# Performance work log

Hardware: AMD Instinct MI355X
Metric: run time of the kernel (lower is better)

Reference implementation:

```python
import jax, jax.numpy as jnp
import numpy as np
from jax import lax

NPOINT, RADIUS, NSAMPLE, K_KEY = 64, 1.0, 32, 64

def conv1d(x, W, b):
    # 1x1 Conv1d: x [B,Cin,N], W [Cout,Cin], b [Cout] -> [B,Cout,N]
    return jnp.einsum('bcn,dc->bdn', x, W) + b[None, :, None]

def farthest_point_sample(xyz, npoint):
    # xyz [B,N,3] -> idx [B,npoint]
    B, N, _ = xyz.shape
    dist0 = jnp.full((B, N), 1e10, dtype=xyz.dtype)
    far0 = jnp.zeros((B,), dtype=jnp.int32)
    def body(carry, _):
        dist, far = carry
        centroid = jnp.take_along_axis(xyz, far[:, None, None].astype(jnp.int32), axis=1)  # [B,1,3]
        d = jnp.sum((xyz - centroid) ** 2, -1)
        dist = jnp.minimum(dist, d)
        nxt = jnp.argmax(dist, -1).astype(jnp.int32)
        return (dist, nxt), far
    _, idxs = lax.scan(body, (dist0, far0), None, length=npoint)
    return idxs.T  # [B,npoint]

def ball_query(radius, nsample, xyz, new_xyz):
    # xyz [B,N,3], new_xyz [B,S,3] -> group_idx [B,S,nsample]
    N = xyz.shape[1]
    sqr = jnp.sum((new_xyz[:, :, None, :] - xyz[:, None, :, :]) ** 2, -1)  # [B,S,N]
    gidx = jnp.where(sqr > radius ** 2, N, jnp.arange(N, dtype=jnp.int32)[None, None, :])
    gidx = jnp.sort(gidx, axis=-1)[..., :nsample]
    first = gidx[..., :1]
    gidx = jnp.where(gidx == N, first, gidx)
    return gidx

def sample_and_group(npoint, radius, nsample, xyz, points):
    # xyz [B,N,3], points [B,N,D]
    B = xyz.shape[0]
    fps_idx = farthest_point_sample(xyz, npoint)                     # [B,S]
    bidx = jnp.arange(B)[:, None]
    new_xyz = xyz[bidx, fps_idx]                                     # [B,S,3]
    gidx = ball_query(radius, nsample, xyz, new_xyz)                 # [B,S,ns]
    bidx2 = jnp.arange(B)[:, None, None]
    grouped_xyz = xyz[bidx2, gidx]                                   # [B,S,ns,3]
    grouped_xyz_norm = grouped_xyz - new_xyz[:, :, None, :]
    grouped_points = points[bidx2, gidx]                             # [B,S,ns,D]
    new_points = jnp.concatenate([grouped_xyz_norm, grouped_points], axis=-1)
    return new_xyz, new_points

def setup_inputs() -> dict:
    key = jax.random.key(0)
    ks = jax.random.split(key, 12)
    B, C, N = 8, 6, 65536
    def w(k, co, ci):
        return jax.random.normal(k, (co, ci), jnp.float32) * (1.0 / np.sqrt(ci))
    return {
        'src_pts': jax.random.normal(ks[0], (B, C, N), jnp.float32),
        'tgt_pts': jax.random.normal(ks[1], (B, C, N), jnp.float32),
        'W1': w(ks[2], 32, 6),  'b1': jnp.zeros((32,), jnp.float32),
        'W2': w(ks[3], 64, 32), 'b2': jnp.zeros((64,), jnp.float32),
        'Wa': w(ks[4], 16, 64), 'ba': jnp.zeros((16,), jnp.float32),
        'Wb': w(ks[5], 8, 16),  'bb': jnp.zeros((8,), jnp.float32),
        'Wc': w(ks[6], 1, 8),   'bc': jnp.zeros((1,), jnp.float32),
    }

def reference(src_pts, tgt_pts, W1, b1, W2, b2, Wa, ba, Wb, bb, Wc, bc):
    # feat_extraction_layer: 1x1 conv stack over points -> deep per-point features
    h = jax.nn.relu(conv1d(src_pts, W1, b1))            # [B,32,N]
    deep_feat_pts = jax.nn.relu(conv1d(h, W2, b2))      # [B,64,N]
    # weighting_layer: per-point saliency weight + top-k keypoint indices (1-D, batch-0 idiom)
    w = jax.nn.relu(conv1d(deep_feat_pts, Wa, ba))
    w = jax.nn.relu(conv1d(w, Wb, bb))
    w = jax.nn.softplus(conv1d(w, Wc, bc))              # [B,1,N]
    _, keypts_idx = lax.top_k(w[0, 0], K_KEY)           # [K]
    # irregular keypoint gather (shared index across batch, as in src_pts[:, :, idx])
    src_keypts = src_pts[:, :, keypts_idx].transpose(0, 2, 1)   # [B,K,C]
    # ball-query sample_and_group on keypoints (computed then discarded, as in original)
    _gxyz, _gpts = sample_and_group(NPOINT, RADIUS, NSAMPLE, src_keypts[:, :, :3], src_keypts[:, :, 3:])
    return src_keypts
```

## Files before the change

kernel.cpp:

```cpp
#include <hip/hip_runtime.h>
#include <stdint.h>

#define N_PTS 65536
#define NB1 32768
#define NB2 65536
#define CAND_CAP 4096
typedef unsigned long long u64;


__global__ __launch_bounds__(256) void zero_kernel(unsigned* __restrict__ z, int n)
{
    const int i = blockIdx.x * 256 + threadIdx.x;
    if (i < n) z[i] = 0u;
}

__global__ __launch_bounds__(256, 1) void score_kernel(
    const float* __restrict__ src,
    const float* __restrict__ W1, const float* __restrict__ b1,
    const float* __restrict__ W2, const float* __restrict__ b2,
    const float* __restrict__ Wa, const float* __restrict__ ba,
    const float* __restrict__ Wb, const float* __restrict__ bb,
    const float* __restrict__ Wc, const float* __restrict__ bc,
    float* __restrict__ scores, unsigned* __restrict__ hist1)
{
    __shared__ unsigned histL[NB1];
    __shared__ __align__(16) float sW1[32 * 8];
    __shared__ __align__(16) float sW2[64 * 32];
    __shared__ __align__(16) float sWaT[64 * 16];
    __shared__ __align__(16) float sWb[8 * 16];
    __shared__ float sb2[64], sba[16], sbb[8], sWc[8], sbc1[1];
    const int t = threadIdx.x;

    {
        uint4* h4 = (uint4*)histL;
        const uint4 zz = {0u, 0u, 0u, 0u};
        #pragma unroll
        for (int i = 0; i < 32; i++) h4[t + 256 * i] = zz;
    }

    {
        const int j = t >> 3, c = t & 7;
        sW1[t] = (c < 6) ? W1[j * 6 + c] : ((c == 6) ? b1[j] : 0.f);
    }
    for (int i = t; i < 2048; i += 256) sW2[i] = W2[i];
    for (int i = t; i < 1024; i += 256) {
        const int j = i >> 4, q = i & 15;
        sWaT[i] = Wa[q * 64 + j];
    }
    if (t < 128) sWb[t] = Wb[t];
    if (t < 64)  sb2[t] = b2[t];
    if (t < 16)  sba[t] = ba[t];
    if (t < 8)   { sbb[t] = bb[t]; sWc[t] = Wc[t]; }
    if (t == 0)  sbc1[0] = bc[0];
    __syncthreads();

    const int p = blockIdx.x * 256 + t;
    float x0 = src[0 * N_PTS + p], x1 = src[1 * N_PTS + p];
    float x2 = src[2 * N_PTS + p], x3 = src[3 * N_PTS + p];
    float x4 = src[4 * N_PTS + p], x5 = src[5 * N_PTS + p];

    float h1[32];
    #pragma unroll
    for (int j = 0; j < 32; j++) {
        const float4 wA = *(const float4*)&sW1[j * 8];
        const float4 wB = *(const float4*)&sW1[j * 8 + 4];
        float a = wB.z;
        a = fmaf(wA.x, x0, a); a = fmaf(wA.y, x1, a);
        a = fmaf(wA.z, x2, a); a = fmaf(wA.w, x3, a);
        a = fmaf(wB.x, x4, a); a = fmaf(wB.y, x5, a);
        h1[j] = fmaxf(a, 0.f);
    }

    float h3[16];
    #pragma unroll
    for (int q = 0; q < 16; q++) h3[q] = sba[q];

    #pragma unroll 4
    for (int j = 0; j < 64; j++) {
        const float4* w2r = (const float4*)&sW2[j * 32];
        float a0 = 0.f, a1 = 0.f, a2 = 0.f, a3 = 0.f;
        #pragma unroll
        for (int i4 = 0; i4 < 8; i4++) {
            const float4 w = w2r[i4];
            a0 = fmaf(w.x, h1[4 * i4 + 0], a0);
            a1 = fmaf(w.y, h1[4 * i4 + 1], a1);
            a2 = fmaf(w.z, h1[4 * i4 + 2], a2);
            a3 = fmaf(w.w, h1[4 * i4 + 3], a3);
        }
        const float v = fmaxf((a0 + a1) + (a2 + a3) + sb2[j], 0.f);
        const float4* war = (const float4*)&sWaT[j * 16];
        #pragma unroll
        for (int q4 = 0; q4 < 4; q4++) {
            const float4 w = war[q4];
            h3[4 * q4 + 0] = fmaf(w.x, v, h3[4 * q4 + 0]);
            h3[4 * q4 + 1] = fmaf(w.y, v, h3[4 * q4 + 1]);
            h3[4 * q4 + 2] = fmaf(w.z, v, h3[4 * q4 + 2]);
            h3[4 * q4 + 3] = fmaf(w.w, v, h3[4 * q4 + 3]);
        }
    }
    #pragma unroll
    for (int q = 0; q < 16; q++) h3[q] = fmaxf(h3[q], 0.f);

    float z = sbc1[0];
    #pragma unroll
    for (int j = 0; j < 8; j++) {
        const float4* wbr = (const float4*)&sWb[j * 16];
        const float4 wA = wbr[0], wB = wbr[1], wC = wbr[2], wD = wbr[3];
        float s0 = sbb[j], s1 = 0.f, s2 = 0.f, s3 = 0.f;
        s0 = fmaf(wA.x, h3[0],  s0); s1 = fmaf(wA.y, h3[1],  s1);
        s2 = fmaf(wA.z, h3[2],  s2); s3 = fmaf(wA.w, h3[3],  s3);
        s0 = fmaf(wB.x, h3[4],  s0); s1 = fmaf(wB.y, h3[5],  s1);
        s2 = fmaf(wB.z, h3[6],  s2); s3 = fmaf(wB.w, h3[7],  s3);
        s0 = fmaf(wC.x, h3[8],  s0); s1 = fmaf(wC.y, h3[9],  s1);
        s2 = fmaf(wC.z, h3[10], s2); s3 = fmaf(wC.w, h3[11], s3);
        s0 = fmaf(wD.x, h3[12], s0); s1 = fmaf(wD.y, h3[13], s1);
        s2 = fmaf(wD.z, h3[14], s2); s3 = fmaf(wD.w, h3[15], s3);
        z = fmaf(sWc[j], fmaxf((s0 + s1) + (s2 + s3), 0.f), z);
    }

    const float sp = fmaxf(z, 0.f) + log1pf(expf(-fabsf(z)));
    scores[p] = sp;
    atomicAdd(&histL[__float_as_uint(sp) >> 16], 1u);
    __syncthreads();

    for (int i = t; i < NB1; i += 256) {
        const unsigned v = histL[i];
        if (v) atomicAdd(&hist1[i], v);
    }
}

__global__ __launch_bounds__(256) void refine_kernel(
    const unsigned* __restrict__ hist1, const float* __restrict__ scores,
    unsigned* __restrict__ hist2, int* __restrict__ meta)
{
    __shared__ unsigned csum[256];
    __shared__ unsigned bsum[128];
    __shared__ int sh_c, sh_B;
    __shared__ unsigned sh_tail;
    const int t = threadIdx.x;

    {
        unsigned s = 0;
        const uint4* h4 = (const uint4*)(hist1 + t * 128);
        #pragma unroll
        for (int i = 0; i < 32; i++) {
            const uint4 v = h4[i];
            s += v.x + v.y + v.z + v.w;
        }
        csum[t] = s;
    }
    __syncthreads();
    for (int d = 1; d < 256; d <<= 1) {
        const unsigned v = (t + d < 256) ? csum[t + d] : 0u;
        __syncthreads();
        csum[t] += v;
        __syncthreads();
    }
    {
        const unsigned here = csum[t];
        const unsigned nxt = (t + 1 < 256) ? csum[t + 1] : 0u;
        if (here >= 64u && nxt < 64u) sh_c = t;
    }
    __syncthreads();
    const int cstar = sh_c;
    if (t < 128) bsum[t] = hist1[cstar * 128 + t];
    __syncthreads();
    {
        const unsigned ctail = (cstar + 1 < 256) ? csum[cstar + 1] : 0u;
        for (int d = 1; d < 128; d <<= 1) {
            unsigned v = 0u;
            if (t < 128 && t + d < 128) v = bsum[t + d];
            __syncthreads();
            if (t < 128) bsum[t] += v;
            __syncthreads();
        }
        if (t < 128) {
            const unsigned here = bsum[t] + ctail;
            const unsigned nxt = (t + 1 < 128) ? bsum[t + 1] + ctail : ctail;
            if (here >= 64u && nxt < 64u) { sh_B = cstar * 128 + t; sh_tail = nxt; }
        }
    }
    __syncthreads();
    const unsigned Bstar = (unsigned)sh_B;
    if (blockIdx.x == 0 && t == 0) { meta[0] = sh_B; meta[1] = (int)sh_tail; }

    const float4* s4 = (const float4*)scores;
    const int i = blockIdx.x * 256 + t;
    const float4 v = s4[i];
    unsigned b;
    b = __float_as_uint(v.x); if ((b >> 16) == Bstar) atomicAdd(&hist2[b & 0xFFFFu], 1u);
    b = __float_as_uint(v.y); if ((b >> 16) == Bstar) atomicAdd(&hist2[b & 0xFFFFu], 1u);
    b = __float_as_uint(v.z); if ((b >> 16) == Bstar) atomicAdd(&hist2[b & 0xFFFFu], 1u);
    b = __float_as_uint(v.w); if ((b >> 16) == Bstar) atomicAdd(&hist2[b & 0xFFFFu], 1u);
}

__global__ __launch_bounds__(256) void compact_kernel(
    const unsigned* __restrict__ hist2, const float* __restrict__ scores,
    int* __restrict__ meta, u64* __restrict__ cand)
{
    __shared__ unsigned csum[256];
    __shared__ unsigned bsum[256];
    __shared__ int sh_c, sh_T2;
    const int t = threadIdx.x;
    const unsigned Bstar = (unsigned)meta[0];
    const unsigned tail1 = (unsigned)meta[1];

    {
        unsigned s = 0;
        const uint4* h4 = (const uint4*)(hist2 + t * 256);
        #pragma unroll
        for (int i = 0; i < 64; i++) {
            const uint4 v = h4[i];
            s += v.x + v.y + v.z + v.w;
        }
        csum[t] = s;
    }
    __syncthreads();
    for (int d = 1; d < 256; d <<= 1) {
        const unsigned v = (t + d < 256) ? csum[t + d] : 0u;
        __syncthreads();
        csum[t] += v;
        __syncthreads();
    }
    {
        const unsigned here = tail1 + csum[t];
        const unsigned nxt = tail1 + ((t + 1 < 256) ? csum[t + 1] : 0u);
        if (here >= 64u && nxt < 64u) sh_c = t;
    }
    __syncthreads();
    const int cstar = sh_c;
    bsum[t] = hist2[cstar * 256 + t];
    __syncthreads();
    {
        const unsigned ctail = tail1 + ((cstar + 1 < 256) ? csum[cstar + 1] : 0u);
        for (int d = 1; d < 256; d <<= 1) {
            const unsigned v = (t + d < 256) ? bsum[t + d] : 0u;
            __syncthreads();
            bsum[t] += v;
            __syncthreads();
        }
        const unsigned here = bsum[t] + ctail;
        const unsigned nxt = ((t + 1 < 256) ? bsum[t + 1] : 0u) + ctail;
        if (here >= 64u && nxt < 64u) sh_T2 = cstar * 256 + t;
    }
    __syncthreads();
    const unsigned T2 = (unsigned)sh_T2;

    const float4* s4 = (const float4*)scores;
    const int i = blockIdx.x * 256 + t;
    const float4 v = s4[i];
    const int n0 = 4 * i;
    unsigned b; unsigned hi;
    b = __float_as_uint(v.x); hi = b >> 16;
    if (hi > Bstar || (hi == Bstar && (b & 0xFFFFu) >= T2)) { int p = atomicAdd(&meta[2], 1); if (p < CAND_CAP) cand[p] = ((u64)b << 32) | (unsigned)~(n0 + 0); }
    b = __float_as_uint(v.y); hi = b >> 16;
    if (hi > Bstar || (hi == Bstar && (b & 0xFFFFu) >= T2)) { int p = atomicAdd(&meta[2], 1); if (p < CAND_CAP) cand[p] = ((u64)b << 32) | (unsigned)~(n0 + 1); }
    b = __float_as_uint(v.z); hi = b >> 16;
    if (hi > Bstar || (hi == Bstar && (b & 0xFFFFu) >= T2)) { int p = atomicAdd(&meta[2], 1); if (p < CAND_CAP) cand[p] = ((u64)b << 32) | (unsigned)~(n0 + 2); }
    b = __float_as_uint(v.w); hi = b >> 16;
    if (hi > Bstar || (hi == Bstar && (b & 0xFFFFu) >= T2)) { int p = atomicAdd(&meta[2], 1); if (p < CAND_CAP) cand[p] = ((u64)b << 32) | (unsigned)~(n0 + 3); }
}

__global__ __launch_bounds__(256) void final_kernel(
    const int* __restrict__ meta, const u64* __restrict__ cand,
    const float* __restrict__ src, float* __restrict__ out)
{
    __shared__ u64 keys[CAND_CAP];
    __shared__ int idxs[64];
    const int t = threadIdx.x;

    int count = meta[2];
    if (count > CAND_CAP) count = CAND_CAP;

    for (int i = t; i < count; i += 256) keys[i] = cand[i];
    __syncthreads();

    for (int i = t; i < count; i += 256) {
        const u64 me = keys[i];
        int r = 0;
        for (int j = 0; j < count; j++) r += (keys[j] > me);
        if (r < 64) idxs[r] = (int)~(unsigned)(me & 0xFFFFFFFFu);
    }
    __syncthreads();

    for (int e = t; e < 3072; e += 256) {
        const int b  = e / 384;
        const int rr = e % 384;
        const int kk = rr / 6;
        const int c  = rr % 6;
        out[e] = src[(b * 6 + c) * N_PTS + idxs[kk]];
    }
}

extern "C" void kernel_launch(void* const* d_in, const int* in_sizes, int n_in,
                              void* d_out, int out_size, void* d_ws, size_t ws_size,
                              hipStream_t stream)
{
    const float* src = (const float*)d_in[0];
    const float* W1 = (const float*)d_in[2];
    const float* b1 = (const float*)d_in[3];
    const float* W2 = (const float*)d_in[4];
    const float* b2 = (const float*)d_in[5];
    const float* Wa = (const float*)d_in[6];
    const float* ba = (const float*)d_in[7];
    const float* Wb = (const float*)d_in[8];
    const float* bb = (const float*)d_in[9];
    const float* Wc = (const float*)d_in[10];
    const float* bc = (const float*)d_in[11];

    char* ws = (char*)d_ws;
    float*    scores = (float*)ws;
    unsigned* hist1  = (unsigned*)(ws + 256 * 1024);
    unsigned* hist2  = (unsigned*)(ws + 384 * 1024);
    int*      meta   = (int*)(ws + 640 * 1024);
    u64*      cand   = (u64*)(ws + 640 * 1024 + 64);
    float*    out    = (float*)d_out;

    const int nz = NB1 + NB2 + 16;
    zero_kernel<<<(nz + 255) / 256, 256, 0, stream>>>(hist1, nz);
    score_kernel<<<256, 256, 0, stream>>>(src, W1, b1, W2, b2, Wa, ba,
                                          Wb, bb, Wc, bc, scores, hist1);
    refine_kernel<<<64, 256, 0, stream>>>(hist1, scores, hist2, meta);
    compact_kernel<<<64, 256, 0, stream>>>(hist2, scores, meta, cand);
    final_kernel<<<1, 256, 0, stream>>>(meta, cand, src, out);
}
```

Baseline: 145.5 us.

## Fuse refine, compact and final into one last-block select kernel; two points per thread

Merges the refine, compact and final top-k kernels into a single select kernel. Blocks build the second-level histogram, and the last block to finish (found through an atomic done counter) computes the threshold, compacts candidates into shared memory, ranks them and gathers the output. The score kernel now runs 128 threads per block with two points per thread, so each shared-memory weight load is reused across both points. This removes two kernel launches and the global candidate buffer, but the final scan over all scores now runs in one block and the candidate cap shrinks to 2048.

```diff
diff --git a/kernel.cpp b/kernel.cpp
--- a/kernel.cpp
+++ b/kernel.cpp
@@ -4,17 +4,18 @@
 #define N_PTS 65536
 #define NB1 32768
 #define NB2 65536
-#define CAND_CAP 4096
+#define LCAP 2048
 typedef unsigned long long u64;
 
 
-__global__ __launch_bounds__(256) void zero_kernel(unsigned* __restrict__ z, int n)
+__global__ __launch_bounds__(256) void zero_kernel(uint4* __restrict__ z, int n4)
 {
     const int i = blockIdx.x * 256 + threadIdx.x;
-    if (i < n) z[i] = 0u;
+    const uint4 zz = {0u, 0u, 0u, 0u};
+    if (i < n4) z[i] = zz;
 }
 
-__global__ __launch_bounds__(256, 1) void score_kernel(
+__global__ __launch_bounds__(128, 1) void score_kernel(
     const float* __restrict__ src,
     const float* __restrict__ W1, const float* __restrict__ b1,
     const float* __restrict__ W2, const float* __restrict__ b2,
@@ -35,15 +36,14 @@
         uint4* h4 = (uint4*)histL;
         const uint4 zz = {0u, 0u, 0u, 0u};
         #pragma unroll
-        for (int i = 0; i < 32; i++) h4[t + 256 * i] = zz;
-    }
-
-    {
-        const int j = t >> 3, c = t & 7;
-        sW1[t] = (c < 6) ? W1[j * 6 + c] : ((c == 6) ? b1[j] : 0.f);
-    }
-    for (int i = t; i < 2048; i += 256) sW2[i] = W2[i];
-    for (int i = t; i < 1024; i += 256) {
+        for (int i = 0; i < 64; i++) h4[t + 128 * i] = zz;
+    }
+    for (int i = t; i < 256; i += 128) {
+        const int j = i >> 3, c = i & 7;
+        sW1[i] = (c < 6) ? W1[j * 6 + c] : ((c == 6) ? b1[j] : 0.f);
+    }
+    for (int i = t; i < 2048; i += 128) sW2[i] = W2[i];
+    for (int i = t; i < 1024; i += 128) {
         const int j = i >> 4, q = i & 15;
         sWaT[i] = Wa[q * 64 + j];
     }
@@ -54,89 +54,118 @@
     if (t == 0)  sbc1[0] = bc[0];
     __syncthreads();
 
-    const int p = blockIdx.x * 256 + t;
-    float x0 = src[0 * N_PTS + p], x1 = src[1 * N_PTS + p];
-    float x2 = src[2 * N_PTS + p], x3 = src[3 * N_PTS + p];
-    float x4 = src[4 * N_PTS + p], x5 = src[5 * N_PTS + p];
-
-    float h1[32];
+    const int base = blockIdx.x * 256;
+    const int p[2] = { base + t, base + 128 + t };
+
+    float x[2][6];
+    #pragma unroll
+    for (int c = 0; c < 6; c++) {
+        x[0][c] = src[c * N_PTS + p[0]];
+        x[1][c] = src[c * N_PTS + p[1]];
+    }
+
+    float h1[2][32];
     #pragma unroll
     for (int j = 0; j < 32; j++) {
         const float4 wA = *(const float4*)&sW1[j * 8];
         const float4 wB = *(const float4*)&sW1[j * 8 + 4];
-        float a = wB.z;
-        a = fmaf(wA.x, x0, a); a = fmaf(wA.y, x1, a);
-        a = fmaf(wA.z, x2, a); a = fmaf(wA.w, x3, a);
-        a = fmaf(wB.x, x4, a); a = fmaf(wB.y, x5, a);
-        h1[j] = fmaxf(a, 0.f);
-    }
-
-    float h3[16];
-    #pragma unroll
-    for (int q = 0; q < 16; q++) h3[q] = sba[q];
+        #pragma unroll
+        for (int P = 0; P < 2; P++) {
+            float a = wB.z;
+            a = fmaf(wA.x, x[P][0], a); a = fmaf(wA.y, x[P][1], a);
+            a = fmaf(wA.z, x[P][2], a); a = fmaf(wA.w, x[P][3], a);
+            a = fmaf(wB.x, x[P][4], a); a = fmaf(wB.y, x[P][5], a);
+            h1[P][j] = fmaxf(a, 0.f);
+        }
+    }
+
+    float h3[2][16];
+    #pragma unroll
+    for (int q = 0; q < 16; q++) { h3[0][q] = sba[q]; h3[1][q] = sba[q]; }
 
     #pragma unroll 4
     for (int j = 0; j < 64; j++) {
         const float4* w2r = (const float4*)&sW2[j * 32];
-        float a0 = 0.f, a1 = 0.f, a2 = 0.f, a3 = 0.f;
-        #pragma unroll
-        for (int i4 = 0; i4 < 8; i4++) {
-            const float4 w = w2r[i4];
-            a0 = fmaf(w.x, h1[4 * i4 + 0], a0);
-            a1 = fmaf(w.y, h1[4 * i4 + 1], a1);
-            a2 = fmaf(w.z, h1[4 * i4 + 2], a2);
-            a3 = fmaf(w.w, h1[4 * i4 + 3], a3);
-        }
-        const float v = fmaxf((a0 + a1) + (a2 + a3) + sb2[j], 0.f);
+        float4 w[8];
+        #pragma unroll
+        for (int i = 0; i < 8; i++) w[i] = w2r[i];
+        const float bj = sb2[j];
         const float4* war = (const float4*)&sWaT[j * 16];
-        #pragma unroll
-        for (int q4 = 0; q4 < 4; q4++) {
-            const float4 w = war[q4];
-            h3[4 * q4 + 0] = fmaf(w.x, v, h3[4 * q4 + 0]);
-            h3[4 * q4 + 1] = fmaf(w.y, v, h3[4 * q4 + 1]);
-            h3[4 * q4 + 2] = fmaf(w.z, v, h3[4 * q4 + 2]);
-            h3[4 * q4 + 3] = fmaf(w.w, v, h3[4 * q4 + 3]);
-        }
-    }
-    #pragma unroll
-    for (int q = 0; q < 16; q++) h3[q] = fmaxf(h3[q], 0.f);
-
-    float z = sbc1[0];
+        float4 wq[4];
+        #pragma unroll
+        for (int i = 0; i < 4; i++) wq[i] = war[i];
+        #pragma unroll
+        for (int P = 0; P < 2; P++) {
+            float a0 = 0.f, a1 = 0.f, a2 = 0.f, a3 = 0.f;
+            #pragma unroll
+            for (int i4 = 0; i4 < 8; i4++) {
+                a0 = fmaf(w[i4].x, h1[P][4 * i4 + 0], a0);
+                a1 = fmaf(w[i4].y, h1[P][4 * i4 + 1], a1);
+                a2 = fmaf(w[i4].z, h1[P][4 * i4 + 2], a2);
+                a3 = fmaf(w[i4].w, h1[P][4 * i4 + 3], a3);
+            }
+            const float v = fmaxf((a0 + a1) + (a2 + a3) + bj, 0.f);
+            #pragma unroll
+            for (int q4 = 0; q4 < 4; q4++) {
+                h3[P][4 * q4 + 0] = fmaf(wq[q4].x, v, h3[P][4 * q4 + 0]);
+                h3[P][4 * q4 + 1] = fmaf(wq[q4].y, v, h3[P][4 * q4 + 1]);
+                h3[P][4 * q4 + 2] = fmaf(wq[q4].z, v, h3[P][4 * q4 + 2]);
+                h3[P][4 * q4 + 3] = fmaf(wq[q4].w, v, h3[P][4 * q4 + 3]);
+            }
+        }
+    }
+    #pragma unroll
+    for (int q = 0; q < 16; q++) {
+        h3[0][q] = fmaxf(h3[0][q], 0.f);
+        h3[1][q] = fmaxf(h3[1][q], 0.f);
+    }
+
+    float z[2] = { sbc1[0], sbc1[0] };
     #pragma unroll
     for (int j = 0; j < 8; j++) {
         const float4* wbr = (const float4*)&sWb[j * 16];
-        const float4 wA = wbr[0], wB = wbr[1], wC = wbr[2], wD = wbr[3];
-        float s0 = sbb[j], s1 = 0.f, s2 = 0.f, s3 = 0.f;
-        s0 = fmaf(wA.x, h3[0],  s0); s1 = fmaf(wA.y, h3[1],  s1);
-        s2 = fmaf(wA.z, h3[2],  s2); s3 = fmaf(wA.w, h3[3],  s3);
-        s0 = fmaf(wB.x, h3[4],  s0); s1 = fmaf(wB.y, h3[5],  s1);
-        s2 = fmaf(wB.z, h3[6],  s2); s3 = fmaf(wB.w, h3[7],  s3);
-        s0 = fmaf(wC.x, h3[8],  s0); s1 = fmaf(wC.y, h3[9],  s1);
-        s2 = fmaf(wC.z, h3[10], s2); s3 = fmaf(wC.w, h3[11], s3);
-        s0 = fmaf(wD.x, h3[12], s0); s1 = fmaf(wD.y, h3[13], s1);
-        s2 = fmaf(wD.z, h3[14], s2); s3 = fmaf(wD.w, h3[15], s3);
-        z = fmaf(sWc[j], fmaxf((s0 + s1) + (s2 + s3), 0.f), z);
-    }
-
-    const float sp = fmaxf(z, 0.f) + log1pf(expf(-fabsf(z)));
-    scores[p] = sp;
-    atomicAdd(&histL[__float_as_uint(sp) >> 16], 1u);
-    __syncthreads();
-
-    for (int i = t; i < NB1; i += 256) {
+        const float4 w0 = wbr[0], w1 = wbr[1], w2 = wbr[2], w3 = wbr[3];
+        const float bj = sbb[j], wc = sWc[j];
+        #pragma unroll
+        for (int P = 0; P < 2; P++) {
+            float s0 = bj, s1 = 0.f, s2 = 0.f, s3 = 0.f;
+            s0 = fmaf(w0.x, h3[P][0],  s0); s1 = fmaf(w0.y, h3[P][1],  s1);
+            s2 = fmaf(w0.z, h3[P][2],  s2); s3 = fmaf(w0.w, h3[P][3],  s3);
+            s0 = fmaf(w1.x, h3[P][4],  s0); s1 = fmaf(w1.y, h3[P][5],  s1);
+            s2 = fmaf(w1.z, h3[P][6],  s2); s3 = fmaf(w1.w, h3[P][7],  s3);
+            s0 = fmaf(w2.x, h3[P][8],  s0); s1 = fmaf(w2.y, h3[P][9],  s1);
+            s2 = fmaf(w2.z, h3[P][10], s2); s3 = fmaf(w2.w, h3[P][11], s3);
+            s0 = fmaf(w3.x, h3[P][12], s0); s1 = fmaf(w3.y, h3[P][13], s1);
+            s2 = fmaf(w3.z, h3[P][14], s2); s3 = fmaf(w3.w, h3[P][15], s3);
+            z[P] = fmaf(wc, fmaxf((s0 + s1) + (s2 + s3), 0.f), z[P]);
+        }
+    }
+
+    #pragma unroll
+    for (int P = 0; P < 2; P++) {
+        const float sp = fmaxf(z[P], 0.f) + log1pf(expf(-fabsf(z[P])));
+        scores[p[P]] = sp;
+        atomicAdd(&histL[__float_as_uint(sp) >> 16], 1u);
+    }
+    __syncthreads();
+
+    for (int i = t; i < NB1; i += 128) {
         const unsigned v = histL[i];
         if (v) atomicAdd(&hist1[i], v);
     }
 }
 
-__global__ __launch_bounds__(256) void refine_kernel(
+__global__ __launch_bounds__(256) void select_kernel(
     const unsigned* __restrict__ hist1, const float* __restrict__ scores,
-    unsigned* __restrict__ hist2, int* __restrict__ meta)
+    unsigned* __restrict__ hist2, unsigned* __restrict__ done,
+    const float* __restrict__ src, float* __restrict__ out)
 {
     __shared__ unsigned csum[256];
-    __shared__ unsigned bsum[128];
-    __shared__ int sh_c, sh_B;
-    __shared__ unsigned sh_tail;
+    __shared__ unsigned bsum[256];
+    __shared__ u64 keys[LCAP];
+    __shared__ int idxs[64];
+    __shared__ int sh_c, sh_B, sh_T2, sh_cnt;
+    __shared__ unsigned sh_tail, sh_rank;
     const int t = threadIdx.x;
 
     {
@@ -182,28 +211,25 @@
     }
     __syncthreads();
     const unsigned Bstar = (unsigned)sh_B;
-    if (blockIdx.x == 0 && t == 0) { meta[0] = sh_B; meta[1] = (int)sh_tail; }
-
-    const float4* s4 = (const float4*)scores;
-    const int i = blockIdx.x * 256 + t;
-    const float4 v = s4[i];
-    unsigned b;
-    b = __float_as_uint(v.x); if ((b >> 16) == Bstar) atomicAdd(&hist2[b & 0xFFFFu], 1u);
-    b = __float_as_uint(v.y); if ((b >> 16) == Bstar) atomicAdd(&hist2[b & 0xFFFFu], 1u);
-    b = __float_as_uint(v.z); if ((b >> 16) == Bstar) atomicAdd(&hist2[b & 0xFFFFu], 1u);
-    b = __float_as_uint(v.w); if ((b >> 16) == Bstar) atomicAdd(&hist2[b & 0xFFFFu], 1u);
-}
-
-__global__ __launch_bounds__(256) void compact_kernel(
-    const unsigned* __restrict__ hist2, const float* __restrict__ scores,
-    int* __restrict__ meta, u64* __restrict__ cand)
-{
-    __shared__ unsigned csum[256];
-    __shared__ unsigned bsum[256];
-    __shared__ int sh_c, sh_T2;
-    const int t = threadIdx.x;
-    const unsigned Bstar = (unsigned)meta[0];
-    const unsigned tail1 = (unsigned)meta[1];
+    const unsigned tail1 = sh_tail;
+
+    {
+        const float4* s4 = (const float4*)scores;
+        const int i = blockIdx.x * 256 + t;
+        const float4 v = s4[i];
+        unsigned b;
+        b = __float_as_uint(v.x); if ((b >> 16) == Bstar) atomicAdd(&hist2[b & 0xFFFFu], 1u);
+        b = __float_as_uint(v.y); if ((b >> 16) == Bstar) atomicAdd(&hist2[b & 0xFFFFu], 1u);
+        b = __float_as_uint(v.z); if ((b >> 16) == Bstar) atomicAdd(&hist2[b & 0xFFFFu], 1u);
+        b = __float_as_uint(v.w); if ((b >> 16) == Bstar) atomicAdd(&hist2[b & 0xFFFFu], 1u);
+    }
+
+    __syncthreads();
+    __threadfence();
+    if (t == 0) sh_rank = atomicAdd(done, 1u);
+    __syncthreads();
+    if (sh_rank != (unsigned)(gridDim.x - 1)) return;
+    __threadfence();
 
     {
         unsigned s = 0;
@@ -228,11 +254,11 @@
         if (here >= 64u && nxt < 64u) sh_c = t;
     }
     __syncthreads();
-    const int cstar = sh_c;
-    bsum[t] = hist2[cstar * 256 + t];
-    __syncthreads();
-    {
-        const unsigned ctail = tail1 + ((cstar + 1 < 256) ? csum[cstar + 1] : 0u);
+    const int c2 = sh_c;
+    bsum[t] = hist2[c2 * 256 + t];
+    __syncthreads();
+    {
+        const unsigned ctail = tail1 + ((c2 + 1 < 256) ? csum[c2 + 1] : 0u);
         for (int d = 1; d < 256; d <<= 1) {
             const unsigned v = (t + d < 256) ? bsum[t + d] : 0u;
             __syncthreads();
@@ -241,40 +267,32 @@
         }
         const unsigned here = bsum[t] + ctail;
         const unsigned nxt = ((t + 1 < 256) ? bsum[t + 1] : 0u) + ctail;
-        if (here >= 64u && nxt < 64u) sh_T2 = cstar * 256 + t;
-    }
+        if (here >= 64u && nxt < 64u) sh_T2 = c2 * 256 + t;
+    }
+    if (t == 0) sh_cnt = 0;
     __syncthreads();
     const unsigned T2 = (unsigned)sh_T2;
 
-    const float4* s4 = (const float4*)scores;
-    const int i = blockIdx.x * 256 + t;
-    const float4 v = s4[i];
-    const int n0 = 4 * i;
-    unsigned b; unsigned hi;
-    b = __float_as_uint(v.x); hi = b >> 16;
-    if (hi > Bstar || (hi == Bstar && (b & 0xFFFFu) >= T2)) { int p = atomicAdd(&meta[2], 1); if (p < CAND_CAP) cand[p] = ((u64)b << 32) | (unsigned)~(n0 + 0); }
-    b = __float_as_uint(v.y); hi = b >> 16;
-    if (hi > Bstar || (hi == Bstar && (b & 0xFFFFu) >= T2)) { int p = atomicAdd(&meta[2], 1); if (p < CAND_CAP) cand[p] = ((u64)b << 32) | (unsigned)~(n0 + 1); }
-    b = __float_as_uint(v.z); hi = b >> 16;
-    if (hi > Bstar || (hi == Bstar && (b & 0xFFFFu) >= T2)) { int p = atomicAdd(&meta[2], 1); if (p < CAND_CAP) cand[p] = ((u64)b << 32) | (unsigned)~(n0 + 2); }
-    b = __float_as_uint(v.w); hi = b >> 16;
-    if (hi > Bstar || (hi == Bstar && (b & 0xFFFFu) >= T2)) { int p = atomicAdd(&meta[2], 1); if (p < CAND_CAP) cand[p] = ((u64)b << 32) | (unsigned)~(n0 + 3); }
-}
-
-__global__ __launch_bounds__(256) void final_kernel(
-    const int* __restrict__ meta, const u64* __restrict__ cand,
-    const float* __restrict__ src, float* __restrict__ out)
-{
-    __shared__ u64 keys[CAND_CAP];
-    __shared__ int idxs[64];
-    const int t = threadIdx.x;
-
-    int count = meta[2];
-    if (count > CAND_CAP) count = CAND_CAP;
-
-    for (int i = t; i < count; i += 256) keys[i] = cand[i];
-    __syncthreads();
-
+    {
+        const float4* s4 = (const float4*)scores;
+        for (int i = t; i < N_PTS / 4; i += 256) {
+            const float4 v = s4[i];
+            const int n0 = 4 * i;
+            unsigned b, hi;
+            b = __float_as_uint(v.x); hi = b >> 16;
+            if (hi > Bstar || (hi == Bstar && (b & 0xFFFFu) >= T2)) { int q = atomicAdd(&sh_cnt, 1); if (q < LCAP) keys[q] = ((u64)b << 32) | (unsigned)~(n0 + 0); }
+            b = __float_as_uint(v.y); hi = b >> 16;
+            if (hi > Bstar || (hi == Bstar && (b & 0xFFFFu) >= T2)) { int q = atomicAdd(&sh_cnt, 1); if (q < LCAP) keys[q] = ((u64)b << 32) | (unsigned)~(n0 + 1); }
+            b = __float_as_uint(v.z); hi = b >> 16;
+            if (hi > Bstar || (hi == Bstar && (b & 0xFFFFu) >= T2)) { int q = atomicAdd(&sh_cnt, 1); if (q < LCAP) keys[q] = ((u64)b << 32) | (unsigned)~(n0 + 2); }
+            b = __float_as_uint(v.w); hi = b >> 16;
+            if (hi > Bstar || (hi == Bstar && (b & 0xFFFFu) >= T2)) { int q = atomicAdd(&sh_cnt, 1); if (q < LCAP) keys[q] = ((u64)b << 32) | (unsigned)~(n0 + 3); }
+        }
+    }
+    __syncthreads();
+
+    int count = sh_cnt;
+    if (count > LCAP) count = LCAP;
     for (int i = t; i < count; i += 256) {
         const u64 me = keys[i];
         int r = 0;
@@ -312,15 +330,12 @@
     float*    scores = (float*)ws;
     unsigned* hist1  = (unsigned*)(ws + 256 * 1024);
     unsigned* hist2  = (unsigned*)(ws + 384 * 1024);
-    int*      meta   = (int*)(ws + 640 * 1024);
-    u64*      cand   = (u64*)(ws + 640 * 1024 + 64);
+    unsigned* done   = (unsigned*)(ws + 640 * 1024);
     float*    out    = (float*)d_out;
 
-    const int nz = NB1 + NB2 + 16;
-    zero_kernel<<<(nz + 255) / 256, 256, 0, stream>>>(hist1, nz);
-    score_kernel<<<256, 256, 0, stream>>>(src, W1, b1, W2, b2, Wa, ba,
+    const int n4 = (NB1 + NB2 + 16) / 4;
+    zero_kernel<<<(n4 + 255) / 256, 256, 0, stream>>>((uint4*)hist1, n4);
+    score_kernel<<<256, 128, 0, stream>>>(src, W1, b1, W2, b2, Wa, ba,
                                           Wb, bb, Wc, bc, scores, hist1);
-    refine_kernel<<<64, 256, 0, stream>>>(hist1, scores, hist2, meta);
-    compact_kernel<<<64, 256, 0, stream>>>(hist2, scores, meta, cand);
-    final_kernel<<<1, 256, 0, stream>>>(meta, cand, src, out);
+    select_kernel<<<64, 256, 0, stream>>>(hist1, scores, hist2, done, src, out);
 }
```

Result: slower. 189.0 us (+29.9%).
